# Kernel tuning notes

Hardware: AMD Instinct MI355X
Metric: run time of the kernel (lower is better)

Reference implementation:

```python
import jax, jax.numpy as jnp
import numpy as np

NU, NB, NI = 100000, 50000, 100000   # users, bundles, items
D = 64                                # embedding dim
L = 3                                 # num propagation layers
NNZ = 2000000                         # sparse graph nonzeros
BATCH = 8192
LEAKY = 0.2
N_UB = NU + NB                        # rows of Graph
N_IU = NI + NU                        # cols of Graph (filter dim)


def setup_inputs() -> dict:
    key = jax.random.key(0)
    ks = jax.random.split(key, 8)
    emb_u = 0.1 * jax.random.normal(ks[0], (NU, D), dtype=jnp.float32)
    emb_b = 0.1 * jax.random.normal(ks[1], (NB, D), dtype=jnp.float32)
    filter_w = jax.random.normal(ks[2], (L, N_IU), dtype=jnp.float32)
    graph_vals = jax.random.uniform(ks[3], (NNZ,), dtype=jnp.float32)
    graph_rows = jax.random.randint(ks[4], (NNZ,), 0, N_UB, dtype=jnp.int32)
    graph_cols = jax.random.randint(ks[5], (NNZ,), 0, N_IU, dtype=jnp.int32)
    u_idx = jax.random.randint(ks[6], (BATCH,), 0, NU, dtype=jnp.int32)
    b_idx = jax.random.randint(ks[7], (BATCH, 2), 0, NB, dtype=jnp.int32)
    return {"emb_u": emb_u, "emb_b": emb_b, "filter_w": filter_w,
            "graph_vals": graph_vals, "graph_rows": graph_rows,
            "graph_cols": graph_cols, "u_idx": u_idx, "b_idx": b_idx}


def _spmm(vals, src, dst, x, n_out):
    # out[dst] += vals * x[src]; x: [n_src, D] -> [n_out, D]
    return jax.ops.segment_sum(vals[:, None] * x[src], dst, num_segments=n_out)


def reference(emb_u, emb_b, filter_w, graph_vals, graph_rows, graph_cols, u_idx, b_idx):
    filt = jax.nn.leaky_relu(filter_w, LEAKY)        # [L, N_IU]
    x = jnp.concatenate([emb_u, emb_b], axis=0)      # [N_UB, D]
    acc = x                                          # running sum of layer embeddings
    for l in range(L):
        y = _spmm(graph_vals, graph_rows, graph_cols, x, N_IU)   # Graph.T @ x
        y = y * filt[l][:, None]                                  # diagonal filter scale
        x = _spmm(graph_vals, graph_cols, graph_rows, y, N_UB)   # Graph @ y
        acc = acc + x
    final = acc / (L + 1)                            # mean over layer buffer
    users, bundles = final[:NU], final[NU:]
    u = users[u_idx]                                 # [B, D]
    b = bundles[b_idx]                               # [B, 2, D]
    rating = jnp.einsum('bkd,bd->bk', b, u)          # [B, 2]
    loss = jnp.mean(jax.nn.softplus(rating[:, 1] - rating[:, 0]))
    l2 = 0.5 * (jnp.sum(emb_u ** 2) + jnp.sum(emb_b ** 2)) / emb_u.shape[0]
    return jnp.stack([loss, l2])
```

## Files before the change

### kernel.cpp

```cpp
#include <hip/hip_runtime.h>
#include <math.h>

#define NU 100000
#define NB 50000
#define NI 100000
#define D 64
#define NLAYER 3
#define NNZ 2000000
#define BATCH 8192
#define LEAKY 0.2f
#define N_UB (NU + NB)
#define N_IU (NI + NU)

#define VSCALE 16383.f

#define WBITS 10
#define WSZ 1024
#define NWC ((N_IU + WSZ - 1) / WSZ)
#define NWR ((N_UB + WSZ - 1) / WSZ)
#define NWIN (NWC + NWR)
#define CAPC 11264
#define CAPR 15360
#define LCAP 15360
#define EPB 8192
#define NBLK_B ((NNZ + EPB - 1) / EPB)
#define CONCAT_BLKS 512
#define GBLK 384
#define NCOLB ((N_IU + 15) / 16)
#define NROWB ((N_UB + 15) / 16)
#define GAB ((3 * BATCH) / 16)

typedef unsigned long long u64;
typedef float v2f __attribute__((ext_vector_type(2)));

__device__ __forceinline__ unsigned pack_fp8x4(float a, float b, float c,
                                               float d) {
  int lo = __builtin_amdgcn_cvt_pk_fp8_f32(a, b, 0, false);
  int pk = __builtin_amdgcn_cvt_pk_fp8_f32(c, d, lo, true);
  return (unsigned)pk;
}
__device__ __forceinline__ void unpack_fp8x4(unsigned w, float f[4]) {
  v2f lo = __builtin_amdgcn_cvt_pk_f32_fp8((int)w, false);
  v2f hi = __builtin_amdgcn_cvt_pk_f32_fp8((int)w, true);
  f[0] = lo[0];
  f[1] = lo[1];
  f[2] = hi[0];
  f[3] = hi[1];
}

__global__ __launch_bounds__(1024) void bucket_concat_kernel(
    const int* __restrict__ rows, const int* __restrict__ cols,
    const float* __restrict__ vals, int* __restrict__ gcurC,
    int* __restrict__ gcurR, u64* __restrict__ bufC, u64* __restrict__ bufR,
    const float* __restrict__ emb_u, const float* __restrict__ emb_b,
    unsigned* __restrict__ x, float* __restrict__ out,
    const int* __restrict__ u_idx, const int* __restrict__ b_idx,
    float* __restrict__ uacc, float* __restrict__ bacc) {
  __shared__ int cntw[NWIN];
  __shared__ int basew[NWIN];
  __shared__ float fsum[16];
  int blk = blockIdx.x;
  int t = threadIdx.x;

  if (blk >= NBLK_B + CONCAT_BLKS) {
    int i = (blk - NBLK_B - CONCAT_BLKS) * 64 + (t >> 4);
    int g = t & 15;
    const float* srcrow;
    float* dst;
    if (i < BATCH) {
      srcrow = emb_u + (size_t)u_idx[i] * D;
      dst = uacc + (size_t)i * D;
    } else {
      int j = i - BATCH;
      srcrow = emb_b + (size_t)b_idx[j] * D;
      dst = bacc + (size_t)j * D;
    }
    *(float4*)&dst[4 * g] = *(const float4*)&srcrow[4 * g];
    return;
  }

  if (blk >= NBLK_B) {
    const int total4 = (N_UB * D) / 4;
    const int nu4 = (NU * D) / 4;
    float sq = 0.f;
    for (int i = (blk - NBLK_B) * 1024 + t; i < total4;
         i += CONCAT_BLKS * 1024) {
      float4 v = (i < nu4) ? ((const float4*)emb_u)[i]
                           : ((const float4*)emb_b)[i - nu4];
      sq += v.x * v.x + v.y * v.y + v.z * v.z + v.w * v.w;
      x[i] = pack_fp8x4(v.x, v.y, v.z, v.w);
    }
    for (int off = 32; off; off >>= 1) sq += __shfl_down(sq, off);
    if ((t & 63) == 0) fsum[t >> 6] = sq;
    __syncthreads();
    if (t == 0) {
      float s = 0.f;
      for (int k = 0; k < 16; ++k) s += fsum[k];
      atomicAdd(&out[1], s * (0.5f / (float)NU));
    }
    return;
  }

  if (t < NWIN) cntw[t] = 0;
  __syncthreads();
  int e0 = blk * EPB;
  int e1 = e0 + EPB;
  if (e1 > NNZ) e1 = NNZ;
  for (int e = e0 + t; e < e1; e += 1024) {
    int c = cols[e];
    int r = rows[e];
    atomicAdd(&cntw[c >> WBITS], 1);
    atomicAdd(&cntw[NWC + (r >> WBITS)], 1);
  }
  __syncthreads();
  if (t < NWC)
    basew[t] = atomicAdd(&gcurC[t], cntw[t]);
  else if (t < NWIN)
    basew[t] = atomicAdd(&gcurR[t - NWC], cntw[t]);
  __syncthreads();
  if (t < NWIN) cntw[t] = 0;
  __syncthreads();
  for (int e = e0 + t; e < e1; e += 1024) {
    int c = cols[e];
    int r = rows[e];
    unsigned q = __float2uint_rn(vals[e] * VSCALE);
    int wc = c >> WBITS;
    int wr = r >> WBITS;
    int oc = atomicAdd(&cntw[wc], 1);
    u64 recC = ((u64)((q << 18) | (unsigned)r) << WBITS) |
               (unsigned)(c & (WSZ - 1));
    bufC[(size_t)wc * CAPC + basew[wc] + oc] = recC;
    int orr = atomicAdd(&cntw[NWC + wr], 1);
    u64 recR = ((u64)((q << 18) | (unsigned)c) << WBITS) |
               (unsigned)(r & (WSZ - 1));
    bufR[(size_t)wr * CAPR + basew[NWC + wr] + orr] = recR;
  }
}

__global__ __launch_bounds__(1024) void csr_sort_kernel(
    const u64* __restrict__ bufC, const u64* __restrict__ bufR,
    const int* __restrict__ gcurC, const int* __restrict__ gcurR,
    unsigned* __restrict__ ec, unsigned* __restrict__ er,
    int* __restrict__ ptrc, int* __restrict__ ptrr) {
  __shared__ u64 recs[LCAP];
  __shared__ int lcnt[WSZ];
  __shared__ int wsum[16];
  __shared__ int wbase_s;
  int blk = blockIdx.x;
  int t = threadIdx.x;

  bool cside = blk < NWC;
  int win = cside ? blk : blk - NWC;
  const u64* buf = cside ? bufC + (size_t)win * CAPC : bufR + (size_t)win * CAPR;
  const int* gsz = cside ? gcurC : gcurR;
  int nwin = cside ? NWC : NWR;
  int nnode = cside ? N_IU : N_UB;
  unsigned* eo = cside ? ec : er;
  int* ptr = cside ? ptrc : ptrr;
  int cnt = gsz[win];
  if (cnt > LCAP) cnt = LCAP;
  if (t == 0) wbase_s = 0;
  lcnt[t] = 0;
  __syncthreads();
  if (t < win) atomicAdd(&wbase_s, gsz[t]);
  for (int i = t; i < cnt; i += 1024) recs[i] = buf[i];
  __syncthreads();
  int winbase = wbase_s;
  for (int i = t; i < cnt; i += 1024)
    atomicAdd(&lcnt[(int)(recs[i] & (WSZ - 1))], 1);
  __syncthreads();
  int a = lcnt[t];
  int lane = t & 63, wid = t >> 6;
  int v = a;
#pragma unroll
  for (int off = 1; off < 64; off <<= 1) {
    int n = __shfl_up(v, off);
    if (lane >= off) v += n;
  }
  if (lane == 63) wsum[wid] = v;
  __syncthreads();
  if (t == 0) {
    int run = 0;
    for (int k = 0; k < 16; ++k) {
      int tmp = wsum[k];
      wsum[k] = run;
      run += tmp;
    }
  }
  __syncthreads();
  int excl = v - a + wsum[wid];
  lcnt[t] = excl;
  int g = win * WSZ + t;
  if (g < nnode) ptr[g] = winbase + excl;
  if (t == 0 && win == nwin - 1) ptr[nnode] = NNZ;
  __syncthreads();
  for (int i = t; i < cnt; i += 1024) {
    u64 rec = recs[i];
    int pos = winbase + atomicAdd(&lcnt[(int)(rec & (WSZ - 1))], 1);
    eo[pos] = (unsigned)(rec >> WBITS);
  }
}

__global__ __launch_bounds__(256) void spmm_col_kernel(
    const int* __restrict__ ptrc, const unsigned* __restrict__ ec,
    const unsigned* __restrict__ x, const float* __restrict__ filt,
    unsigned* __restrict__ y, const int* __restrict__ u_idx,
    const int* __restrict__ b_idx, float* __restrict__ uacc,
    float* __restrict__ bacc) {
  int blk = blockIdx.x;
  if (blk >= NCOLB) {
    int t = threadIdx.x;
    int i = (blk - NCOLB) * 16 + (t >> 4);
    int g = t & 15;
    int src;
    float* dst;
    if (i < BATCH) {
      src = u_idx[i];
      dst = &uacc[(size_t)i * D];
    } else {
      int j = i - BATCH;
      src = NU + b_idx[j];
      dst = &bacc[(size_t)j * D];
    }
    float f4[4];
    unpack_fp8x4(x[(size_t)src * 16 + g], f4);
    float4* dp = (float4*)&dst[4 * g];
    float4 d = *dp;
    d.x += f4[0];
    d.y += f4[1];
    d.z += f4[2];
    d.w += f4[3];
    *dp = d;
    return;
  }
  int wv = blk * 4 + (threadIdx.x >> 6);
  int lane = threadIdx.x & 63;
  int g = lane & 15;
  int c = wv * 4 + (lane >> 4);
  if (c >= N_IU) return;
  int e = ptrc[c], e2 = ptrc[c + 1];
  float a0 = 0.f, a1 = 0.f, a2 = 0.f, a3 = 0.f;
  for (; e + 8 <= e2; e += 8) {
    unsigned p0 = __builtin_nontemporal_load(&ec[e]);
    unsigned p1 = __builtin_nontemporal_load(&ec[e + 1]);
    unsigned p2 = __builtin_nontemporal_load(&ec[e + 2]);
    unsigned p3 = __builtin_nontemporal_load(&ec[e + 3]);
    unsigned p4 = __builtin_nontemporal_load(&ec[e + 4]);
    unsigned p5 = __builtin_nontemporal_load(&ec[e + 5]);
    unsigned p6 = __builtin_nontemporal_load(&ec[e + 6]);
    unsigned p7 = __builtin_nontemporal_load(&ec[e + 7]);
    unsigned w0 = x[(size_t)(p0 & 0x3FFFFu) * 16 + g];
    unsigned w1 = x[(size_t)(p1 & 0x3FFFFu) * 16 + g];
    unsigned w2 = x[(size_t)(p2 & 0x3FFFFu) * 16 + g];
    unsigned w3 = x[(size_t)(p3 & 0x3FFFFu) * 16 + g];
    unsigned w4 = x[(size_t)(p4 & 0x3FFFFu) * 16 + g];
    unsigned w5 = x[(size_t)(p5 & 0x3FFFFu) * 16 + g];
    unsigned w6 = x[(size_t)(p6 & 0x3FFFFu) * 16 + g];
    unsigned w7 = x[(size_t)(p7 & 0x3FFFFu) * 16 + g];
    float f0[4], f1[4], f2[4], f3[4], f4_[4], f5[4], f6[4], f7[4];
    unpack_fp8x4(w0, f0);
    unpack_fp8x4(w1, f1);
    unpack_fp8x4(w2, f2);
    unpack_fp8x4(w3, f3);
    unpack_fp8x4(w4, f4_);
    unpack_fp8x4(w5, f5);
    unpack_fp8x4(w6, f6);
    unpack_fp8x4(w7, f7);
    float v0 = (float)(p0 >> 18), v1 = (float)(p1 >> 18);
    float v2 = (float)(p2 >> 18), v3 = (float)(p3 >> 18);
    float v4 = (float)(p4 >> 18), v5 = (float)(p5 >> 18);
    float v6 = (float)(p6 >> 18), v7 = (float)(p7 >> 18);
    a0 += v0 * f0[0] + v1 * f1[0] + v2 * f2[0] + v3 * f3[0] + v4 * f4_[0] +
          v5 * f5[0] + v6 * f6[0] + v7 * f7[0];
    a1 += v0 * f0[1] + v1 * f1[1] + v2 * f2[1] + v3 * f3[1] + v4 * f4_[1] +
          v5 * f5[1] + v6 * f6[1] + v7 * f7[1];
    a2 += v0 * f0[2] + v1 * f1[2] + v2 * f2[2] + v3 * f3[2] + v4 * f4_[2] +
          v5 * f5[2] + v6 * f6[2] + v7 * f7[2];
    a3 += v0 * f0[3] + v1 * f1[3] + v2 * f2[3] + v3 * f3[3] + v4 * f4_[3] +
          v5 * f5[3] + v6 * f6[3] + v7 * f7[3];
  }
  for (; e + 4 <= e2; e += 4) {
    unsigned p0 = __builtin_nontemporal_load(&ec[e]);
    unsigned p1 = __builtin_nontemporal_load(&ec[e + 1]);
    unsigned p2 = __builtin_nontemporal_load(&ec[e + 2]);
    unsigned p3 = __builtin_nontemporal_load(&ec[e + 3]);
    unsigned w0 = x[(size_t)(p0 & 0x3FFFFu) * 16 + g];
    unsigned w1 = x[(size_t)(p1 & 0x3FFFFu) * 16 + g];
    unsigned w2 = x[(size_t)(p2 & 0x3FFFFu) * 16 + g];
    unsigned w3 = x[(size_t)(p3 & 0x3FFFFu) * 16 + g];
    float f0[4], f1[4], f2[4], f3[4];
    unpack_fp8x4(w0, f0);
    unpack_fp8x4(w1, f1);
    unpack_fp8x4(w2, f2);
    unpack_fp8x4(w3, f3);
    float v0 = (float)(p0 >> 18), v1 = (float)(p1 >> 18);
    float v2 = (float)(p2 >> 18), v3 = (float)(p3 >> 18);
    a0 += v0 * f0[0] + v1 * f1[0] + v2 * f2[0] + v3 * f3[0];
    a1 += v0 * f0[1] + v1 * f1[1] + v2 * f2[1] + v3 * f3[1];
    a2 += v0 * f0[2] + v1 * f1[2] + v2 * f2[2] + v3 * f3[2];
    a3 += v0 * f0[3] + v1 * f1[3] + v2 * f2[3] + v3 * f3[3];
  }
  for (; e < e2; ++e) {
    unsigned p = __builtin_nontemporal_load(&ec[e]);
    unsigned w = x[(size_t)(p & 0x3FFFFu) * 16 + g];
    float f4[4];
    unpack_fp8x4(w, f4);
    float v = (float)(p >> 18);
    a0 += v * f4[0];
    a1 += v * f4[1];
    a2 += v * f4[2];
    a3 += v * f4[3];
  }
  float fw = filt[c];
  float f = (fw > 0.f ? fw : LEAKY * fw) * (1.f / VSCALE);
  y[(size_t)c * 16 + g] = pack_fp8x4(a0 * f, a1 * f, a2 * f, a3 * f);
}

__global__ __launch_bounds__(256) void spmm_row_kernel(
    const int* __restrict__ ptrr, const unsigned* __restrict__ er,
    const unsigned* __restrict__ y, unsigned* __restrict__ x) {
  int wv = blockIdx.x * 4 + (threadIdx.x >> 6);
  int lane = threadIdx.x & 63;
  int g = lane & 15;
  int r = wv * 4 + (lane >> 4);
  if (r >= N_UB) return;
  int e = ptrr[r], e2 = ptrr[r + 1];
  float a0 = 0.f, a1 = 0.f, a2 = 0.f, a3 = 0.f;
  for (; e + 8 <= e2; e += 8) {
    unsigned p0 = __builtin_nontemporal_load(&er[e]);
    unsigned p1 = __builtin_nontemporal_load(&er[e + 1]);
    unsigned p2 = __builtin_nontemporal_load(&er[e + 2]);
    unsigned p3 = __builtin_nontemporal_load(&er[e + 3]);
    unsigned p4 = __builtin_nontemporal_load(&er[e + 4]);
    unsigned p5 = __builtin_nontemporal_load(&er[e + 5]);
    unsigned p6 = __builtin_nontemporal_load(&er[e + 6]);
    unsigned p7 = __builtin_nontemporal_load(&er[e + 7]);
    unsigned w0 = y[(size_t)(p0 & 0x3FFFFu) * 16 + g];
    unsigned w1 = y[(size_t)(p1 & 0x3FFFFu) * 16 + g];
    unsigned w2 = y[(size_t)(p2 & 0x3FFFFu) * 16 + g];
    unsigned w3 = y[(size_t)(p3 & 0x3FFFFu) * 16 + g];
    unsigned w4 = y[(size_t)(p4 & 0x3FFFFu) * 16 + g];
    unsigned w5 = y[(size_t)(p5 & 0x3FFFFu) * 16 + g];
    unsigned w6 = y[(size_t)(p6 & 0x3FFFFu) * 16 + g];
    unsigned w7 = y[(size_t)(p7 & 0x3FFFFu) * 16 + g];
    float f0[4], f1[4], f2[4], f3[4], f4_[4], f5[4], f6[4], f7[4];
    unpack_fp8x4(w0, f0);
    unpack_fp8x4(w1, f1);
    unpack_fp8x4(w2, f2);
    unpack_fp8x4(w3, f3);
    unpack_fp8x4(w4, f4_);
    unpack_fp8x4(w5, f5);
    unpack_fp8x4(w6, f6);
    unpack_fp8x4(w7, f7);
    float v0 = (float)(p0 >> 18), v1 = (float)(p1 >> 18);
    float v2 = (float)(p2 >> 18), v3 = (float)(p3 >> 18);
    float v4 = (float)(p4 >> 18), v5 = (float)(p5 >> 18);
    float v6 = (float)(p6 >> 18), v7 = (float)(p7 >> 18);
    a0 += v0 * f0[0] + v1 * f1[0] + v2 * f2[0] + v3 * f3[0] + v4 * f4_[0] +
          v5 * f5[0] + v6 * f6[0] + v7 * f7[0];
    a1 += v0 * f0[1] + v1 * f1[1] + v2 * f2[1] + v3 * f3[1] + v4 * f4_[1] +
          v5 * f5[1] + v6 * f6[1] + v7 * f7[1];
    a2 += v0 * f0[2] + v1 * f1[2] + v2 * f2[2] + v3 * f3[2] + v4 * f4_[2] +
          v5 * f5[2] + v6 * f6[2] + v7 * f7[2];
    a3 += v0 * f0[3] + v1 * f1[3] + v2 * f2[3] + v3 * f3[3] + v4 * f4_[3] +
          v5 * f5[3] + v6 * f6[3] + v7 * f7[3];
  }
  for (; e + 4 <= e2; e += 4) {
    unsigned p0 = __builtin_nontemporal_load(&er[e]);
    unsigned p1 = __builtin_nontemporal_load(&er[e + 1]);
    unsigned p2 = __builtin_nontemporal_load(&er[e + 2]);
    unsigned p3 = __builtin_nontemporal_load(&er[e + 3]);
    unsigned w0 = y[(size_t)(p0 & 0x3FFFFu) * 16 + g];
    unsigned w1 = y[(size_t)(p1 & 0x3FFFFu) * 16 + g];
    unsigned w2 = y[(size_t)(p2 & 0x3FFFFu) * 16 + g];
    unsigned w3 = y[(size_t)(p3 & 0x3FFFFu) * 16 + g];
    float f0[4], f1[4], f2[4], f3[4];
    unpack_fp8x4(w0, f0);
    unpack_fp8x4(w1, f1);
    unpack_fp8x4(w2, f2);
    unpack_fp8x4(w3, f3);
    float v0 = (float)(p0 >> 18), v1 = (float)(p1 >> 18);
    float v2 = (float)(p2 >> 18), v3 = (float)(p3 >> 18);
    a0 += v0 * f0[0] + v1 * f1[0] + v2 * f2[0] + v3 * f3[0];
    a1 += v0 * f0[1] + v1 * f1[1] + v2 * f2[1] + v3 * f3[1];
    a2 += v0 * f0[2] + v1 * f1[2] + v2 * f2[2] + v3 * f3[2];
    a3 += v0 * f0[3] + v1 * f1[3] + v2 * f2[3] + v3 * f3[3];
  }
  for (; e < e2; ++e) {
    unsigned p = __builtin_nontemporal_load(&er[e]);
    unsigned w = y[(size_t)(p & 0x3FFFFu) * 16 + g];
    float f4[4];
    unpack_fp8x4(w, f4);
    float v = (float)(p >> 18);
    a0 += v * f4[0];
    a1 += v * f4[1];
    a2 += v * f4[2];
    a3 += v * f4[3];
  }
  const float s = 1.f / VSCALE;
  x[(size_t)r * 16 + g] = pack_fp8x4(a0 * s, a1 * s, a2 * s, a3 * s);
}

__global__ __launch_bounds__(256) void spmm_gather_last_kernel(
    const int* __restrict__ ptrr, const unsigned* __restrict__ er,
    const unsigned* __restrict__ y, const int* __restrict__ u_idx,
    const int* __restrict__ b_idx, float* __restrict__ uacc,
    float* __restrict__ bacc) {
  int wv = blockIdx.x * 4 + (threadIdx.x >> 6);
  int lane = threadIdx.x & 63;
  int g = lane & 15;
  int i = wv * 4 + (lane >> 4);
  if (i >= 3 * BATCH) return;
  int row;
  float* dst;
  if (i < BATCH) {
    row = u_idx[i];
    dst = &uacc[(size_t)i * D];
  } else {
    int j = i - BATCH;
    row = NU + b_idx[j];
    dst = &bacc[(size_t)j * D];
  }
  int e = ptrr[row], e2 = ptrr[row + 1];
  float a0 = 0.f, a1 = 0.f, a2 = 0.f, a3 = 0.f;
  for (; e < e2; ++e) {
    unsigned p = er[e];
    unsigned w = y[(size_t)(p & 0x3FFFFu) * 16 + g];
    float f4[4];
    unpack_fp8x4(w, f4);
    float v = (float)(p >> 18);
    a0 += v * f4[0];
    a1 += v * f4[1];
    a2 += v * f4[2];
    a3 += v * f4[3];
  }
  const float s = 1.f / VSCALE;
  float4* dp = (float4*)&dst[4 * g];
  float4 d = *dp;
  d.x += a0 * s;
  d.y += a1 * s;
  d.z += a2 * s;
  d.w += a3 * s;
  *dp = d;
}

__global__ __launch_bounds__(256) void loss_kernel(
    const float* __restrict__ uacc, const float* __restrict__ bacc,
    float* __restrict__ out) {
  __shared__ float bsum[8];
  int t = threadIdx.x;
  int slot = t >> 5;
  int sub = t & 31;
  float acc = 0.f;
  for (int i = blockIdx.x * 8 + slot; i < BATCH; i += gridDim.x * 8) {
    float2 u = *(const float2*)&uacc[(size_t)i * D + 2 * sub];
    float2 b0 = *(const float2*)&bacc[(size_t)(2 * i) * D + 2 * sub];
    float2 b1 = *(const float2*)&bacc[(size_t)(2 * i + 1) * D + 2 * sub];
    float tt = (u.x * (b1.x - b0.x) + u.y * (b1.y - b0.y)) * (1.f / 16.f);
    for (int off = 16; off; off >>= 1) tt += __shfl_down(tt, off, 32);
    if (sub == 0) {
      float z = tt;
      acc += z > 0.f ? z + log1pf(expf(-z)) : log1pf(expf(z));
    }
  }
  if (sub == 0) bsum[slot] = acc;
  __syncthreads();
  if (t == 0) {
    float s = 0.f;
    for (int k = 0; k < 8; ++k) s += bsum[k];
    atomicAdd(&out[0], s * (1.f / (float)BATCH));
  }
}

extern "C" void kernel_launch(void* const* d_in, const int* in_sizes, int n_in,
                              void* d_out, int out_size, void* d_ws,
                              size_t ws_size, hipStream_t stream) {
  const float* emb_u = (const float*)d_in[0];
  const float* emb_b = (const float*)d_in[1];
  const float* filter_w = (const float*)d_in[2];
  const float* vals = (const float*)d_in[3];
  const int* rows = (const int*)d_in[4];
  const int* cols = (const int*)d_in[5];
  const int* u_idx = (const int*)d_in[6];
  const int* b_idx = (const int*)d_in[7];
  float* out = (float*)d_out;

  char* base = (char*)d_ws;
  u64* bufC = (u64*)base;
  u64* bufR = bufC + (size_t)NWC * CAPC;
  unsigned* yH = (unsigned*)base;
  char* after = base + ((size_t)NWC * CAPC + (size_t)NWR * CAPR) * 8;
  unsigned* xA = (unsigned*)after;
  unsigned* ec = xA + (size_t)N_UB * 16;
  unsigned* er = ec + NNZ;
  int* ptrc = (int*)(er + NNZ);
  int* ptrr = ptrc + (N_IU + 1);
  int* gcurC = ptrr + (N_UB + 1);
  int* gcurR = gcurC + NWC;
  float* uacc = (float*)(gcurR + NWR);
  float* bacc = uacc + (size_t)BATCH * D;

  hipMemsetAsync(out, 0, 2 * sizeof(float), stream);
  hipMemsetAsync(gcurC, 0, NWIN * sizeof(int), stream);

  bucket_concat_kernel<<<NBLK_B + CONCAT_BLKS + GBLK, 1024, 0, stream>>>(
      rows, cols, vals, gcurC, gcurR, bufC, bufR, emb_u, emb_b, xA, out, u_idx,
      b_idx, uacc, bacc);
  csr_sort_kernel<<<NWIN, 1024, 0, stream>>>(bufC, bufR, gcurC, gcurR, ec, er,
                                             ptrc, ptrr);

  for (int l = 0; l < NLAYER; ++l) {
    int colgrid = NCOLB + (l > 0 ? GAB : 0);
    spmm_col_kernel<<<colgrid, 256, 0, stream>>>(
        ptrc, ec, xA, filter_w + (size_t)l * N_IU, yH, u_idx, b_idx, uacc,
        bacc);
    if (l < NLAYER - 1) {
      spmm_row_kernel<<<NROWB, 256, 0, stream>>>(ptrr, er, yH, xA);
    } else {
      spmm_gather_last_kernel<<<(3 * BATCH + 15) / 16, 256, 0, stream>>>(
          ptrr, er, yH, u_idx, b_idx, uacc, bacc);
    }
  }

  loss_kernel<<<256, 256, 0, stream>>>(uacc, bacc, out);
}
```

Baseline: 331.9 us.

## Split fp8 embeddings into four dimension planes and parallelize SpMM over planes

```diff
diff --git a/kernel.cpp b/kernel.cpp
--- a/kernel.cpp
+++ b/kernel.cpp
@@ -13,6 +13,9 @@
 #define N_IU (NI + NU)
 
 #define VSCALE 16383.f
+
+#define PLX ((size_t)N_UB * 4)
+#define PLY ((size_t)N_IU * 4)
 
 #define WBITS 10
 #define WSZ 1024
@@ -88,7 +91,10 @@
       float4 v = (i < nu4) ? ((const float4*)emb_u)[i]
                            : ((const float4*)emb_b)[i - nu4];
       sq += v.x * v.x + v.y * v.y + v.z * v.z + v.w * v.w;
-      x[i] = pack_fp8x4(v.x, v.y, v.z, v.w);
+      int n = i >> 4;
+      int dg = i & 15;
+      x[(size_t)(dg >> 2) * PLX + (size_t)n * 4 + (dg & 3)] =
+          pack_fp8x4(v.x, v.y, v.z, v.w);
     }
     for (int off = 32; off; off >>= 1) sq += __shfl_down(sq, off);
     if ((t & 63) == 0) fsum[t >> 6] = sq;
@@ -208,10 +214,10 @@
     const int* __restrict__ b_idx, float* __restrict__ uacc,
     float* __restrict__ bacc) {
   int blk = blockIdx.x;
-  if (blk >= NCOLB) {
+  if (blk >= 4 * NCOLB) {
     int t = threadIdx.x;
-    int i = (blk - NCOLB) * 16 + (t >> 4);
-    int g = t & 15;
+    int i = (blk - 4 * NCOLB) * 16 + (t >> 4);
+    int sub = t & 15;
     int src;
     float* dst;
     if (i < BATCH) {
@@ -223,8 +229,8 @@
       dst = &bacc[(size_t)j * D];
     }
     float f4[4];
-    unpack_fp8x4(x[(size_t)src * 16 + g], f4);
-    float4* dp = (float4*)&dst[4 * g];
+    unpack_fp8x4(x[(size_t)(sub >> 2) * PLX + (size_t)src * 4 + (sub & 3)], f4);
+    float4* dp = (float4*)&dst[4 * sub];
     float4 d = *dp;
     d.x += f4[0];
     d.y += f4[1];
@@ -233,76 +239,35 @@
     *dp = d;
     return;
   }
-  int wv = blk * 4 + (threadIdx.x >> 6);
+  int q = blk / NCOLB;
+  int cb = blk % NCOLB;
   int lane = threadIdx.x & 63;
-  int g = lane & 15;
-  int c = wv * 4 + (lane >> 4);
+  int sub16 = lane & 15;
+  int quad = sub16 >> 2;
+  int ql = sub16 & 3;
+  int c = (cb * 4 + (threadIdx.x >> 6)) * 4 + (lane >> 4);
   if (c >= N_IU) return;
-  int e = ptrc[c], e2 = ptrc[c + 1];
+  const unsigned* xq = x + (size_t)q * PLX;
+  int e2 = ptrc[c + 1];
+  int e = ptrc[c] + quad;
   float a0 = 0.f, a1 = 0.f, a2 = 0.f, a3 = 0.f;
-  for (; e + 8 <= e2; e += 8) {
-    unsigned p0 = __builtin_nontemporal_load(&ec[e]);
-    unsigned p1 = __builtin_nontemporal_load(&ec[e + 1]);
-    unsigned p2 = __builtin_nontemporal_load(&ec[e + 2]);
-    unsigned p3 = __builtin_nontemporal_load(&ec[e + 3]);
-    unsigned p4 = __builtin_nontemporal_load(&ec[e + 4]);
-    unsigned p5 = __builtin_nontemporal_load(&ec[e + 5]);
-    unsigned p6 = __builtin_nontemporal_load(&ec[e + 6]);
-    unsigned p7 = __builtin_nontemporal_load(&ec[e + 7]);
-    unsigned w0 = x[(size_t)(p0 & 0x3FFFFu) * 16 + g];
-    unsigned w1 = x[(size_t)(p1 & 0x3FFFFu) * 16 + g];
-    unsigned w2 = x[(size_t)(p2 & 0x3FFFFu) * 16 + g];
-    unsigned w3 = x[(size_t)(p3 & 0x3FFFFu) * 16 + g];
-    unsigned w4 = x[(size_t)(p4 & 0x3FFFFu) * 16 + g];
-    unsigned w5 = x[(size_t)(p5 & 0x3FFFFu) * 16 + g];
-    unsigned w6 = x[(size_t)(p6 & 0x3FFFFu) * 16 + g];
-    unsigned w7 = x[(size_t)(p7 & 0x3FFFFu) * 16 + g];
-    float f0[4], f1[4], f2[4], f3[4], f4_[4], f5[4], f6[4], f7[4];
-    unpack_fp8x4(w0, f0);
-    unpack_fp8x4(w1, f1);
-    unpack_fp8x4(w2, f2);
-    unpack_fp8x4(w3, f3);
-    unpack_fp8x4(w4, f4_);
-    unpack_fp8x4(w5, f5);
-    unpack_fp8x4(w6, f6);
-    unpack_fp8x4(w7, f7);
-    float v0 = (float)(p0 >> 18), v1 = (float)(p1 >> 18);
-    float v2 = (float)(p2 >> 18), v3 = (float)(p3 >> 18);
-    float v4 = (float)(p4 >> 18), v5 = (float)(p5 >> 18);
-    float v6 = (float)(p6 >> 18), v7 = (float)(p7 >> 18);
-    a0 += v0 * f0[0] + v1 * f1[0] + v2 * f2[0] + v3 * f3[0] + v4 * f4_[0] +
-          v5 * f5[0] + v6 * f6[0] + v7 * f7[0];
-    a1 += v0 * f0[1] + v1 * f1[1] + v2 * f2[1] + v3 * f3[1] + v4 * f4_[1] +
-          v5 * f5[1] + v6 * f6[1] + v7 * f7[1];
-    a2 += v0 * f0[2] + v1 * f1[2] + v2 * f2[2] + v3 * f3[2] + v4 * f4_[2] +
-          v5 * f5[2] + v6 * f6[2] + v7 * f7[2];
-    a3 += v0 * f0[3] + v1 * f1[3] + v2 * f2[3] + v3 * f3[3] + v4 * f4_[3] +
-          v5 * f5[3] + v6 * f6[3] + v7 * f7[3];
-  }
-  for (; e + 4 <= e2; e += 4) {
-    unsigned p0 = __builtin_nontemporal_load(&ec[e]);
-    unsigned p1 = __builtin_nontemporal_load(&ec[e + 1]);
-    unsigned p2 = __builtin_nontemporal_load(&ec[e + 2]);
-    unsigned p3 = __builtin_nontemporal_load(&ec[e + 3]);
-    unsigned w0 = x[(size_t)(p0 & 0x3FFFFu) * 16 + g];
-    unsigned w1 = x[(size_t)(p1 & 0x3FFFFu) * 16 + g];
-    unsigned w2 = x[(size_t)(p2 & 0x3FFFFu) * 16 + g];
-    unsigned w3 = x[(size_t)(p3 & 0x3FFFFu) * 16 + g];
-    float f0[4], f1[4], f2[4], f3[4];
-    unpack_fp8x4(w0, f0);
-    unpack_fp8x4(w1, f1);
-    unpack_fp8x4(w2, f2);
-    unpack_fp8x4(w3, f3);
-    float v0 = (float)(p0 >> 18), v1 = (float)(p1 >> 18);
-    float v2 = (float)(p2 >> 18), v3 = (float)(p3 >> 18);
-    a0 += v0 * f0[0] + v1 * f1[0] + v2 * f2[0] + v3 * f3[0];
-    a1 += v0 * f0[1] + v1 * f1[1] + v2 * f2[1] + v3 * f3[1];
-    a2 += v0 * f0[2] + v1 * f1[2] + v2 * f2[2] + v3 * f3[2];
-    a3 += v0 * f0[3] + v1 * f1[3] + v2 * f2[3] + v3 * f3[3];
-  }
-  for (; e < e2; ++e) {
+  for (; e + 4 < e2; e += 8) {
+    unsigned pA = __builtin_nontemporal_load(&ec[e]);
+    unsigned pB = __builtin_nontemporal_load(&ec[e + 4]);
+    unsigned wA = xq[(size_t)(pA & 0x3FFFFu) * 4 + ql];
+    unsigned wB = xq[(size_t)(pB & 0x3FFFFu) * 4 + ql];
+    float fA[4], fB[4];
+    unpack_fp8x4(wA, fA);
+    unpack_fp8x4(wB, fB);
+    float vA = (float)(pA >> 18), vB = (float)(pB >> 18);
+    a0 += vA * fA[0] + vB * fB[0];
+    a1 += vA * fA[1] + vB * fB[1];
+    a2 += vA * fA[2] + vB * fB[2];
+    a3 += vA * fA[3] + vB * fB[3];
+  }
+  if (e < e2) {
     unsigned p = __builtin_nontemporal_load(&ec[e]);
-    unsigned w = x[(size_t)(p & 0x3FFFFu) * 16 + g];
+    unsigned w = xq[(size_t)(p & 0x3FFFFu) * 4 + ql];
     float f4[4];
     unpack_fp8x4(w, f4);
     float v = (float)(p >> 18);
@@ -311,84 +276,56 @@
     a2 += v * f4[2];
     a3 += v * f4[3];
   }
-  float fw = filt[c];
-  float f = (fw > 0.f ? fw : LEAKY * fw) * (1.f / VSCALE);
-  y[(size_t)c * 16 + g] = pack_fp8x4(a0 * f, a1 * f, a2 * f, a3 * f);
+  a0 += __shfl_xor(a0, 4);
+  a1 += __shfl_xor(a1, 4);
+  a2 += __shfl_xor(a2, 4);
+  a3 += __shfl_xor(a3, 4);
+  a0 += __shfl_xor(a0, 8);
+  a1 += __shfl_xor(a1, 8);
+  a2 += __shfl_xor(a2, 8);
+  a3 += __shfl_xor(a3, 8);
+  if (quad == 0) {
+    float fw = filt[c];
+    float f = (fw > 0.f ? fw : LEAKY * fw) * (1.f / VSCALE);
+    __builtin_nontemporal_store(
+        pack_fp8x4(a0 * f, a1 * f, a2 * f, a3 * f),
+        &y[(size_t)q * PLY + (size_t)c * 4 + ql]);
+  }
 }
 
 __global__ __launch_bounds__(256) void spmm_row_kernel(
     const int* __restrict__ ptrr, const unsigned* __restrict__ er,
     const unsigned* __restrict__ y, unsigned* __restrict__ x) {
-  int wv = blockIdx.x * 4 + (threadIdx.x >> 6);
+  int blk = blockIdx.x;
+  int q = blk / NROWB;
+  int rb = blk % NROWB;
   int lane = threadIdx.x & 63;
-  int g = lane & 15;
-  int r = wv * 4 + (lane >> 4);
+  int sub16 = lane & 15;
+  int quad = sub16 >> 2;
+  int ql = sub16 & 3;
+  int r = (rb * 4 + (threadIdx.x >> 6)) * 4 + (lane >> 4);
   if (r >= N_UB) return;
-  int e = ptrr[r], e2 = ptrr[r + 1];
+  const unsigned* yq = y + (size_t)q * PLY;
+  int e2 = ptrr[r + 1];
+  int e = ptrr[r] + quad;
   float a0 = 0.f, a1 = 0.f, a2 = 0.f, a3 = 0.f;
-  for (; e + 8 <= e2; e += 8) {
-    unsigned p0 = __builtin_nontemporal_load(&er[e]);
-    unsigned p1 = __builtin_nontemporal_load(&er[e + 1]);
-    unsigned p2 = __builtin_nontemporal_load(&er[e + 2]);
-    unsigned p3 = __builtin_nontemporal_load(&er[e + 3]);
-    unsigned p4 = __builtin_nontemporal_load(&er[e + 4]);
-    unsigned p5 = __builtin_nontemporal_load(&er[e + 5]);
-    unsigned p6 = __builtin_nontemporal_load(&er[e + 6]);
-    unsigned p7 = __builtin_nontemporal_load(&er[e + 7]);
-    unsigned w0 = y[(size_t)(p0 & 0x3FFFFu) * 16 + g];
-    unsigned w1 = y[(size_t)(p1 & 0x3FFFFu) * 16 + g];
-    unsigned w2 = y[(size_t)(p2 & 0x3FFFFu) * 16 + g];
-    unsigned w3 = y[(size_t)(p3 & 0x3FFFFu) * 16 + g];
-    unsigned w4 = y[(size_t)(p4 & 0x3FFFFu) * 16 + g];
-    unsigned w5 = y[(size_t)(p5 & 0x3FFFFu) * 16 + g];
-    unsigned w6 = y[(size_t)(p6 & 0x3FFFFu) * 16 + g];
-    unsigned w7 = y[(size_t)(p7 & 0x3FFFFu) * 16 + g];
-    float f0[4], f1[4], f2[4], f3[4], f4_[4], f5[4], f6[4], f7[4];
-    unpack_fp8x4(w0, f0);
-    unpack_fp8x4(w1, f1);
-    unpack_fp8x4(w2, f2);
-    unpack_fp8x4(w3, f3);
-    unpack_fp8x4(w4, f4_);
-    unpack_fp8x4(w5, f5);
-    unpack_fp8x4(w6, f6);
-    unpack_fp8x4(w7, f7);
-    float v0 = (float)(p0 >> 18), v1 = (float)(p1 >> 18);
-    float v2 = (float)(p2 >> 18), v3 = (float)(p3 >> 18);
-    float v4 = (float)(p4 >> 18), v5 = (float)(p5 >> 18);
-    float v6 = (float)(p6 >> 18), v7 = (float)(p7 >> 18);
-    a0 += v0 * f0[0] + v1 * f1[0] + v2 * f2[0] + v3 * f3[0] + v4 * f4_[0] +
-          v5 * f5[0] + v6 * f6[0] + v7 * f7[0];
-    a1 += v0 * f0[1] + v1 * f1[1] + v2 * f2[1] + v3 * f3[1] + v4 * f4_[1] +
-          v5 * f5[1] + v6 * f6[1] + v7 * f7[1];
-    a2 += v0 * f0[2] + v1 * f1[2] + v2 * f2[2] + v3 * f3[2] + v4 * f4_[2] +
-          v5 * f5[2] + v6 * f6[2] + v7 * f7[2];
-    a3 += v0 * f0[3] + v1 * f1[3] + v2 * f2[3] + v3 * f3[3] + v4 * f4_[3] +
-          v5 * f5[3] + v6 * f6[3] + v7 * f7[3];
-  }
-  for (; e + 4 <= e2; e += 4) {
-    unsigned p0 = __builtin_nontemporal_load(&er[e]);
-    unsigned p1 = __builtin_nontemporal_load(&er[e + 1]);
-    unsigned p2 = __builtin_nontemporal_load(&er[e + 2]);
-    unsigned p3 = __builtin_nontemporal_load(&er[e + 3]);
-    unsigned w0 = y[(size_t)(p0 & 0x3FFFFu) * 16 + g];
-    unsigned w1 = y[(size_t)(p1 & 0x3FFFFu) * 16 + g];
-    unsigned w2 = y[(size_t)(p2 & 0x3FFFFu) * 16 + g];
-    unsigned w3 = y[(size_t)(p3 & 0x3FFFFu) * 16 + g];
-    float f0[4], f1[4], f2[4], f3[4];
-    unpack_fp8x4(w0, f0);
-    unpack_fp8x4(w1, f1);
-    unpack_fp8x4(w2, f2);
-    unpack_fp8x4(w3, f3);
-    float v0 = (float)(p0 >> 18), v1 = (float)(p1 >> 18);
-    float v2 = (float)(p2 >> 18), v3 = (float)(p3 >> 18);
-    a0 += v0 * f0[0] + v1 * f1[0] + v2 * f2[0] + v3 * f3[0];
-    a1 += v0 * f0[1] + v1 * f1[1] + v2 * f2[1] + v3 * f3[1];
-    a2 += v0 * f0[2] + v1 * f1[2] + v2 * f2[2] + v3 * f3[2];
-    a3 += v0 * f0[3] + v1 * f1[3] + v2 * f2[3] + v3 * f3[3];
-  }
-  for (; e < e2; ++e) {
+  for (; e + 4 < e2; e += 8) {
+    unsigned pA = __builtin_nontemporal_load(&er[e]);
+    unsigned pB = __builtin_nontemporal_load(&er[e + 4]);
+    unsigned wA = yq[(size_t)(pA & 0x3FFFFu) * 4 + ql];
+    unsigned wB = yq[(size_t)(pB & 0x3FFFFu) * 4 + ql];
+    float fA[4], fB[4];
+    unpack_fp8x4(wA, fA);
+    unpack_fp8x4(wB, fB);
+    float vA = (float)(pA >> 18), vB = (float)(pB >> 18);
+    a0 += vA * fA[0] + vB * fB[0];
+    a1 += vA * fA[1] + vB * fB[1];
+    a2 += vA * fA[2] + vB * fB[2];
+    a3 += vA * fA[3] + vB * fB[3];
+  }
+  if (e < e2) {
     unsigned p = __builtin_nontemporal_load(&er[e]);
-    unsigned w = y[(size_t)(p & 0x3FFFFu) * 16 + g];
+    unsigned w = yq[(size_t)(p & 0x3FFFFu) * 4 + ql];
     float f4[4];
     unpack_fp8x4(w, f4);
     float v = (float)(p >> 18);
@@ -397,8 +334,20 @@
     a2 += v * f4[2];
     a3 += v * f4[3];
   }
-  const float s = 1.f / VSCALE;
-  x[(size_t)r * 16 + g] = pack_fp8x4(a0 * s, a1 * s, a2 * s, a3 * s);
+  a0 += __shfl_xor(a0, 4);
+  a1 += __shfl_xor(a1, 4);
+  a2 += __shfl_xor(a2, 4);
+  a3 += __shfl_xor(a3, 4);
+  a0 += __shfl_xor(a0, 8);
+  a1 += __shfl_xor(a1, 8);
+  a2 += __shfl_xor(a2, 8);
+  a3 += __shfl_xor(a3, 8);
+  if (quad == 0) {
+    const float s = 1.f / VSCALE;
+    __builtin_nontemporal_store(
+        pack_fp8x4(a0 * s, a1 * s, a2 * s, a3 * s),
+        &x[(size_t)q * PLX + (size_t)r * 4 + ql]);
+  }
 }
 
 __global__ __launch_bounds__(256) void spmm_gather_last_kernel(
@@ -408,9 +357,11 @@
     float* __restrict__ bacc) {
   int wv = blockIdx.x * 4 + (threadIdx.x >> 6);
   int lane = threadIdx.x & 63;
-  int g = lane & 15;
+  int sub16 = lane & 15;
   int i = wv * 4 + (lane >> 4);
   if (i >= 3 * BATCH) return;
+  const unsigned* yp = y + (size_t)(sub16 >> 2) * PLY;
+  int ql = sub16 & 3;
   int row;
   float* dst;
   if (i < BATCH) {
@@ -425,7 +376,7 @@
   float a0 = 0.f, a1 = 0.f, a2 = 0.f, a3 = 0.f;
   for (; e < e2; ++e) {
     unsigned p = er[e];
-    unsigned w = y[(size_t)(p & 0x3FFFFu) * 16 + g];
+    unsigned w = yp[(size_t)(p & 0x3FFFFu) * 4 + ql];
     float f4[4];
     unpack_fp8x4(w, f4);
     float v = (float)(p >> 18);
@@ -435,7 +386,7 @@
     a3 += v * f4[3];
   }
   const float s = 1.f / VSCALE;
-  float4* dp = (float4*)&dst[4 * g];
+  float4* dp = (float4*)&dst[4 * sub16];
   float4 d = *dp;
   d.x += a0 * s;
   d.y += a1 * s;
@@ -491,7 +442,7 @@
   unsigned* yH = (unsigned*)base;
   char* after = base + ((size_t)NWC * CAPC + (size_t)NWR * CAPR) * 8;
   unsigned* xA = (unsigned*)after;
-  unsigned* ec = xA + (size_t)N_UB * 16;
+  unsigned* ec = xA + (size_t)4 * PLX;
   unsigned* er = ec + NNZ;
   int* ptrc = (int*)(er + NNZ);
   int* ptrr = ptrc + (N_IU + 1);
@@ -510,12 +461,12 @@
                                              ptrc, ptrr);
 
   for (int l = 0; l < NLAYER; ++l) {
-    int colgrid = NCOLB + (l > 0 ? GAB : 0);
+    int colgrid = 4 * NCOLB + (l > 0 ? GAB : 0);
     spmm_col_kernel<<<colgrid, 256, 0, stream>>>(
         ptrc, ec, xA, filter_w + (size_t)l * N_IU, yH, u_idx, b_idx, uacc,
         bacc);
     if (l < NLAYER - 1) {
-      spmm_row_kernel<<<NROWB, 256, 0, stream>>>(ptrr, er, yH, xA);
+      spmm_row_kernel<<<4 * NROWB, 256, 0, stream>>>(ptrr, er, yH, xA);
     } else {
       spmm_gather_last_kernel<<<(3 * BATCH + 15) / 16, 256, 0, stream>>>(
           ptrr, er, yH, u_idx, b_idx, uacc, bacc);
```

Result: slower. 559.3 us (+68.5%).
